# Kernel tuning notes

Hardware: AMD Instinct MI355X
Metric: run time of the kernel (lower is better)

## Reference

```python
import jax, jax.numpy as jnp
from jax import lax
import numpy as np

DN = ('NCHW', 'OIHW', 'NCHW')

def _bn(x, g, b):
    # BatchNorm2d in training mode: batch statistics, biased variance, eps=1e-5
    m = jnp.mean(x, axis=(0, 2, 3), keepdims=True)
    v = jnp.var(x, axis=(0, 2, 3), keepdims=True)
    return g[None, :, None, None] * (x - m) * lax.rsqrt(v + 1e-5) + b[None, :, None, None]

def _conv(x, w, b, s, p):
    y = lax.conv_general_dilated(x, w, (s, s), [(p, p), (p, p)], dimension_numbers=DN)
    return y + b[None, :, None, None]

def _convt(x, w, b, s, p):
    # torch ConvTranspose2d weight layout [in, out, k, k]; equivalent to
    # input-dilated conv with flipped, transposed kernel and padding k-1-p.
    k = w.shape[2]
    pp = k - 1 - p
    w2 = jnp.flip(w, (2, 3)).transpose(1, 0, 2, 3)  # [out, in, k, k]
    y = lax.conv_general_dilated(x, w2, (1, 1), [(pp, pp), (pp, pp)],
                                 lhs_dilation=(s, s), dimension_numbers=DN)
    return y + b[None, :, None, None]

def setup_inputs() -> dict:
    key = jax.random.key(0)
    ks = jax.random.split(key, 16)
    f32 = jnp.float32
    def rn(i, shape, s):
        return jax.random.normal(ks[i], shape, f32) * s
    K = 256
    inp = {
        'x': jax.random.normal(ks[0], (128, 3, 64, 64), f32),
        'codebook': jax.random.uniform(ks[1], (256, 256), f32, -1.0 / K, 1.0 / K),
        'e_w1': rn(2, (64, 3, 3, 3), 0.19), 'e_b1': jnp.zeros((64,), f32),
        'e_g1': jnp.ones((64,), f32), 'e_be1': jnp.zeros((64,), f32),
        'e_w2': rn(3, (128, 64, 4, 4), 0.031), 'e_b2': jnp.zeros((128,), f32),
        'e_g2': jnp.ones((128,), f32), 'e_be2': jnp.zeros((128,), f32),
        'e_w3': rn(4, (192, 128, 4, 4), 0.022), 'e_b3': jnp.zeros((192,), f32),
        'e_g3': jnp.ones((192,), f32), 'e_be3': jnp.zeros((192,), f32),
        'e_w4': rn(5, (256, 192, 1, 1), 0.072), 'e_b4': jnp.zeros((256,), f32),
        'd_w1': rn(6, (256, 192, 1, 1), 0.062), 'd_b1': jnp.zeros((192,), f32),
        'd_g1': jnp.ones((192,), f32), 'd_be1': jnp.zeros((192,), f32),
        'd_w2': rn(7, (192, 128, 4, 4), 0.018), 'd_b2': jnp.zeros((128,), f32),
        'd_g2': jnp.ones((128,), f32), 'd_be2': jnp.zeros((128,), f32),
        'd_w3': rn(8, (128, 64, 4, 4), 0.022), 'd_b3': jnp.zeros((64,), f32),
        'd_g3': jnp.ones((64,), f32), 'd_be3': jnp.zeros((64,), f32),
        'd_w4': rn(9, (3, 64, 3, 3), 0.042), 'd_b4': jnp.zeros((3,), f32),
    }
    return inp

def reference(x, codebook,
              e_w1, e_b1, e_g1, e_be1, e_w2, e_b2, e_g2, e_be2,
              e_w3, e_b3, e_g3, e_be3, e_w4, e_b4,
              d_w1, d_b1, d_g1, d_be1, d_w2, d_b2, d_g2, d_be2,
              d_w3, d_b3, d_g3, d_be3, d_w4, d_b4):
    # encoder
    h = jax.nn.relu(_bn(_conv(x, e_w1, e_b1, 1, 1), e_g1, e_be1))
    h = jax.nn.relu(_bn(_conv(h, e_w2, e_b2, 2, 1), e_g2, e_be2))
    h = jax.nn.relu(_bn(_conv(h, e_w3, e_b3, 2, 1), e_g3, e_be3))
    h = _conv(h, e_w4, e_b4, 1, 0)  # [B, 256, 16, 16]
    B, C, H, W = h.shape
    Z = h.transpose(0, 2, 3, 1).reshape(-1, C)  # [N, D]
    # fused cdist via ||a||^2 + ||b||^2 - 2ab (argmin invariant to const offsets)
    d2 = (jnp.sum(Z * Z, axis=1, keepdims=True)
          + jnp.sum(codebook * codebook, axis=1)[None, :]
          - 2.0 * (Z @ codebook.T))  # [N, K]
    j = jnp.argmin(d2, axis=1)
    Wj = codebook[j]  # [N, D]
    loss_commit = jnp.mean(jnp.sum((Z - lax.stop_gradient(Wj)) ** 2, axis=1))
    loss_code = jnp.mean(jnp.sum((lax.stop_gradient(Z) - Wj) ** 2, axis=1))
    hq = Wj.reshape(B, H, W, C).transpose(0, 3, 1, 2)
    # decoder
    g = jax.nn.relu(_bn(_convt(hq, d_w1, d_b1, 1, 0), d_g1, d_be1))
    g = jax.nn.relu(_bn(_convt(g, d_w2, d_b2, 2, 1), d_g2, d_be2))
    g = jax.nn.relu(_bn(_convt(g, d_w3, d_b3, 2, 1), d_g3, d_be3))
    g = _conv(g, d_w4, d_b4, 1, 1)  # [B, 3, 64, 64]
    return g, loss_commit, loss_code
```

## Files before the change

kernel.cpp:

```cpp
#include <hip/hip_runtime.h>

#define TPB 256

typedef __attribute__((ext_vector_type(4))) float v4f;
typedef __attribute__((ext_vector_type(8))) short v8s;

__device__ __forceinline__ float us2f(unsigned int u) {
    union { unsigned int i; float f; } w; w.i = u << 16; return w.f;
}
__device__ __forceinline__ unsigned short f2us(float f) {
    union { float ff; unsigned int i; } w; w.ff = f;
    unsigned int u = w.i;
    return (unsigned short)((u + 0x7fffu + ((u >> 16) & 1u)) >> 16);
}
__device__ __forceinline__ void gl_lds16(const unsigned short* g, unsigned short* l) {
    __builtin_amdgcn_global_load_lds(
        (const __attribute__((address_space(1))) unsigned int*)g,
        (__attribute__((address_space(3))) unsigned int*)l, 16, 0, 0);
}

template<int CIN, int COUT, int KK>
__global__ __launch_bounds__(TPB) void repack_w(
    const float* __restrict__ w, unsigned short* __restrict__ o)
{
    int idx = blockIdx.x * TPB + threadIdx.x;
    if (idx >= KK * COUT * CIN) return;
    int ci = idx % CIN;
    int co = (idx / CIN) % COUT;
    int kk = idx / (CIN * COUT);
    o[idx] = f2us(w[((size_t)co * CIN + ci) * KK + kk]);
}
template<int CIN, int COUT>
__global__ __launch_bounds__(TPB) void repack_wt1(
    const float* __restrict__ w, unsigned short* __restrict__ o)
{
    int idx = blockIdx.x * TPB + threadIdx.x;
    if (idx >= CIN * COUT) return;
    int ci = idx % CIN;
    int co = idx / CIN;
    o[idx] = f2us(w[(size_t)ci * COUT + co]);
}
__global__ __launch_bounds__(TPB) void repack_we1(
    const float* __restrict__ w, unsigned short* __restrict__ o)
{
    int idx = blockIdx.x * TPB + threadIdx.x;
    if (idx >= 64 * 32) return;
    int k = idx & 31, co = idx >> 5;
    o[idx] = (k < 27) ? f2us(w[co * 27 + k]) : (unsigned short)0;
}
__global__ __launch_bounds__(TPB) void repack_wd4(
    const float* __restrict__ w, unsigned short* __restrict__ o)
{
    int idx = blockIdx.x * TPB + threadIdx.x;
    if (idx >= 18 * 512) return;
    int e = idx & 7;
    int lane = (idx >> 3) & 63;
    int kk = idx >> 9;
    int lr = lane & 15, lc = lane >> 4;
    int tap = kk >> 1, half = kk & 1;
    int ci = half * 32 + lc * 8 + e;
    o[idx] = (lr < 3) ? f2us(w[((size_t)lr * 64 + ci) * 9 + tap]) : (unsigned short)0;
}
template<int CIN, int COUT, int NCB>
__global__ __launch_bounds__(TPB) void repack_wf2(
    const float* __restrict__ w, unsigned short* __restrict__ o)
{
    int idx = blockIdx.x * TPB + threadIdx.x;
    if (idx >= 16 * COUT * CIN) return;
    int e = idx & 7;
    int lane = (idx >> 3) & 63;
    int seg8 = (idx >> 9) & 7;
    int u = idx >> 12;
    int cb = u % NCB;
    int tap = u / NCB;
    int lr = lane & 15, lc = lane >> 4;
    int kc = seg8 >> 2, sg = seg8 & 3;
    int co = cb * 64 + sg * 16 + lr;
    int ci = kc * 32 + lc * 8 + e;
    o[idx] = f2us(w[((size_t)co * CIN + ci) * 16 + tap]);
}
template<int CIN, int COUT, int NCB>
__global__ __launch_bounds__(TPB) void repack_wct2(
    const float* __restrict__ w, unsigned short* __restrict__ o)
{
    constexpr int NCI = CIN / 64;
    int idx = blockIdx.x * TPB + threadIdx.x;
    if (idx >= 16 * COUT * CIN) return;
    int e = idx & 7;
    int lane = (idx >> 3) & 63;
    int seg8 = (idx >> 9) & 7;
    int u = idx >> 12;
    int cb = u % NCB;
    int u2 = u / NCB;
    int cc = u2 % NCI;
    int tk = u2 / NCI;
    int kidx = tk & 3, cls = tk >> 2;
    int lr = lane & 15, lc = lane >> 4;
    int kc = seg8 >> 2, sg = seg8 & 3;
    int co = cb * 64 + sg * 16 + lr;
    int ci = cc * 64 + kc * 32 + lc * 8 + e;
    int ohp = cls >> 1, owp = cls & 1;
    int kh = ((ohp + 1) & 1) + 2 * (kidx >> 1);
    int kw = ((owp + 1) & 1) + 2 * (kidx & 1);
    o[idx] = f2us(w[((size_t)ci * COUT + co) * 16 + kh * 4 + kw]);
}

__global__ __launch_bounds__(TPB) void im2col_e1(
    const float* __restrict__ x, unsigned short* __restrict__ A, int N)
{
    int p = blockIdx.x * TPB + threadIdx.x;
    int n = p >> 12, oh = (p >> 6) & 63, ow = p & 63;
    unsigned short row[32];
#pragma unroll
    for (int k = 0; k < 27; k++) {
        int ci = k / 9, tap = k % 9, kh = tap / 3, kw = tap % 3;
        int ih = oh - 1 + kh, iw = ow - 1 + kw;
        float v = ((unsigned)ih < 64u && (unsigned)iw < 64u)
            ? x[(((size_t)n * 3 + ci) * 64 + ih) * 64 + iw] : 0.f;
        row[k] = f2us(v);
    }
#pragma unroll
    for (int k = 27; k < 32; k++) row[k] = 0;
    int4* dst = (int4*)(A + (size_t)p * 32);
    const int4* src = (const int4*)row;
    dst[0] = src[0]; dst[1] = src[1]; dst[2] = src[2]; dst[3] = src[3];
}

__global__ __launch_bounds__(TPB) void e1_gemm(
    const unsigned short* __restrict__ A, const unsigned short* __restrict__ wrep,
    const float* __restrict__ bias, unsigned short* __restrict__ yout,
    float* __restrict__ part, int N)
{
    __shared__ __align__(16) unsigned short Ab[8 * 512];
    __shared__ __align__(16) unsigned short Bb[4 * 512];

    const int t = threadIdx.x, lane = t & 63, wave = t >> 6;
    const int wm = wave >> 1, wn = wave & 1;
    const int m0 = (int)blockIdx.x * 128;
    const int lr = lane & 15, lc = lane >> 4;

    gl_lds16(A + (size_t)(m0 + wave * 16 + lr) * 32 + lc * 8, &Ab[wave * 512]);
    gl_lds16(A + (size_t)(m0 + (wave + 4) * 16 + lr) * 32 + lc * 8, &Ab[(wave + 4) * 512]);
    gl_lds16(wrep + (size_t)(wave * 16 + lr) * 32 + lc * 8, &Bb[wave * 512]);
    __syncthreads();

    v4f acc[4][2];
#pragma unroll
    for (int i = 0; i < 4; i++)
#pragma unroll
        for (int j = 0; j < 2; j++)
#pragma unroll
            for (int r = 0; r < 4; r++) acc[i][j][r] = 0.f;

    v8s a[4], b[2];
#pragma unroll
    for (int i = 0; i < 4; i++)
        a[i] = *(const v8s*)&Ab[(wm * 4 + i) * 512 + lane * 8];
#pragma unroll
    for (int j = 0; j < 2; j++)
        b[j] = *(const v8s*)&Bb[(wn * 2 + j) * 512 + lane * 8];
#pragma unroll
    for (int i = 0; i < 4; i++)
#pragma unroll
        for (int j = 0; j < 2; j++)
            acc[i][j] = __builtin_amdgcn_mfma_f32_16x16x32_bf16(a[i], b[j], acc[i][j], 0, 0, 0);

    float sloc[2], qloc[2];
#pragma unroll
    for (int j = 0; j < 2; j++) { sloc[j] = 0.f; qloc[j] = 0.f; }

#pragma unroll
    for (int i = 0; i < 4; i++) {
        int mr = wm * 64 + i * 16 + (lane >> 4) * 4;
#pragma unroll
        for (int j = 0; j < 2; j++) {
            int col = wn * 32 + j * 16 + (lane & 15);
            float bs = bias[col];
#pragma unroll
            for (int r = 0; r < 4; r++) {
                int row = m0 + mr + r;
                int n = row >> 12, oh = (row >> 6) & 63, ow = row & 63;
                int cls = ((oh & 1) << 1) | (ow & 1);
                size_t crow = ((((size_t)cls * N + n) * 32 + (oh >> 1)) * 32 + (ow >> 1));
                float v = acc[i][j][r] + bs;
                yout[crow * 64 + col] = f2us(v);
                sloc[j] += v;
                qloc[j] += v * v;
            }
        }
    }

    __syncthreads();
    float* red = (float*)Ab;
    for (int i = t; i < 128; i += TPB) red[i] = 0.f;
    __syncthreads();
#pragma unroll
    for (int j = 0; j < 2; j++) {
        float s = sloc[j], qv = qloc[j];
        s += __shfl_xor(s, 16); s += __shfl_xor(s, 32);
        qv += __shfl_xor(qv, 16); qv += __shfl_xor(qv, 32);
        if ((lane >> 4) == 0) {
            int cl = wn * 32 + j * 16 + (lane & 15);
            atomicAdd(&red[cl], s);
            atomicAdd(&red[64 + cl], qv);
        }
    }
    __syncthreads();
    int PB = (int)gridDim.x, pb = (int)blockIdx.x;
    for (int i = t; i < 64; i += TPB) {
        part[(size_t)i * PB + pb] = red[i];
        part[(size_t)(64 + i) * PB + pb] = red[64 + i];
    }
}

template<int CIN, int COUT, int HO, int WO, int NCB>
__global__ __launch_bounds__(TPB) void conv_c(
    const unsigned short* __restrict__ xin, const unsigned short* __restrict__ wrep,
    const float* __restrict__ bias, unsigned short* __restrict__ yout,
    float* __restrict__ part, const unsigned short* __restrict__ zpage, int N)
{
    constexpr int NCI = CIN / 64;
    constexpr int NIT = 16 * NCI;
    __shared__ __align__(16) unsigned short Ab[2][16 * 1024];
    __shared__ __align__(16) unsigned short Bb[2][8 * 512];

    const int t = threadIdx.x, lane = t & 63, wave = t >> 6;
    int gdec = (int)blockIdx.x >> 3, xs = (int)blockIdx.x & 7;
    int cb = 0;
    if (NCB >= 2) { cb = gdec % NCB; gdec /= NCB; }
    const int tile = (gdec << 3) + xs;
    const int m0 = tile * 256;
    const int co0 = cb * 64;
    const int lr = lane & 15, lc = lane >> 4;

    const int jr7 = lane >> 3;
    const int sw = ((lane & 7) ^ jr7) * 8;

    int n_[4], oh_[4], ow0_[4];
#pragma unroll
    for (int q = 0; q < 4; q++) {
        int r0 = m0 + (wave * 4 + q) * 16;
        n_[q] = r0 / (HO * WO);
        int rem = r0 % (HO * WO);
        oh_[q] = rem / WO;
        ow0_[q] = rem % WO;
    }

    v4f acc[4][4];
#pragma unroll
    for (int i = 0; i < 4; i++)
#pragma unroll
        for (int j = 0; j < 4; j++)
#pragma unroll
            for (int r = 0; r < 4; r++) acc[i][j][r] = 0.f;

    auto stage = [&](int it, int buf) {
        const int tap = it / NCI, cc = it % NCI;
        const int kh = tap >> 2, kw = tap & 3;
        const int dcls = (((kh + 1) & 1) << 1) | ((kw + 1) & 1);
        const int dh2 = (kh - 1) >> 1;
        const int dw2 = (kw - 1) >> 1;
#pragma unroll
        for (int q = 0; q < 4; q++) {
            const int ih2 = oh_[q] + dh2;
            const bool ihv = (unsigned)ih2 < (unsigned)HO;
#pragma unroll
            for (int h = 0; h < 2; h++) {
                int iw2 = ow0_[q] + h * 8 + jr7 + dw2;
                bool av = ihv && (unsigned)iw2 < (unsigned)WO;
                size_t ab = ((((size_t)dcls * N + n_[q]) * HO + ih2) * WO + iw2) * CIN;
                const unsigned short* src = av ? xin + ab + cc * 64 + sw : zpage;
                gl_lds16(src, &Ab[buf][(wave * 4 + q) * 1024 + h * 512]);
            }
        }
        const unsigned short* wb = wrep
            + ((size_t)(tap * NCI + cc) * NCB + cb) * 4096;
        gl_lds16(wb + wave * 512 + lane * 8, &Bb[buf][wave * 512]);
        gl_lds16(wb + (4 + wave) * 512 + lane * 8, &Bb[buf][(4 + wave) * 512]);
    };

    auto compute = [&](int it, int buf) {
#pragma unroll
        for (int kc = 0; kc < 2; kc++) {
            v8s a[4], b[4];
#pragma unroll
            for (int i = 0; i < 4; i++)
                a[i] = *(const v8s*)&Ab[buf][(wave * 4 + i) * 1024 + lr * 64
                        + ((kc * 32 + lc * 8) ^ ((lr & 7) << 3))];
#pragma unroll
            for (int j = 0; j < 4; j++)
                b[j] = *(const v8s*)&Bb[buf][(kc * 4 + j) * 512 + lane * 8];
#pragma unroll
            for (int i = 0; i < 4; i++)
#pragma unroll
                for (int j = 0; j < 4; j++)
                    acc[i][j] = __builtin_amdgcn_mfma_f32_16x16x32_bf16(a[i], b[j], acc[i][j], 0, 0, 0);
        }
    };

    stage(0, 0);
    __syncthreads();

#pragma unroll
    for (int it = 0; it < NIT; ++it) {
        const int buf = it & 1;
        if (it + 1 < NIT) stage(it + 1, buf ^ 1);
        compute(it, buf);
        __syncthreads();
    }

    float sloc[4], qloc[4];
#pragma unroll
    for (int j = 0; j < 4; j++) { sloc[j] = 0.f; qloc[j] = 0.f; }

#pragma unroll
    for (int i = 0; i < 4; i++) {
        int mr = wave * 64 + i * 16 + (lane >> 4) * 4;
#pragma unroll
        for (int j = 0; j < 4; j++) {
            int col = co0 + j * 16 + (lane & 15);
            float bs = bias[col];
#pragma unroll
            for (int r = 0; r < 4; r++) {
                size_t gi = (size_t)(m0 + mr + r) * COUT + col;
                float v = acc[i][j][r] + bs;
                yout[gi] = f2us(v);
                sloc[j] += v;
                qloc[j] += v * v;
            }
        }
    }

    float* red = (float*)Ab;
    for (int i = t; i < 128; i += TPB) red[i] = 0.f;
    __syncthreads();
#pragma unroll
    for (int j = 0; j < 4; j++) {
        float s = sloc[j], qv = qloc[j];
        s += __shfl_xor(s, 16); s += __shfl_xor(s, 32);
        qv += __shfl_xor(qv, 16); qv += __shfl_xor(qv, 32);
        if ((lane >> 4) == 0) {
            int cl = j * 16 + (lane & 15);
            atomicAdd(&red[cl], s);
            atomicAdd(&red[64 + cl], qv);
        }
    }
    __syncthreads();
    const int TILES = (N * HO * WO) >> 8;
    const int pb = tile;
    for (int i = t; i < 64; i += TPB) {
        part[(size_t)(co0 + i) * TILES + pb] = red[i];
        part[(size_t)(COUT + co0 + i) * TILES + pb] = red[64 + i];
    }
}

template<int CIN, int COUT, int HIN, int WIN, int K, int S, int P, int BN,
         int OUTM, int NYB>
__global__ __launch_bounds__(TPB) void conv_mfma(
    const unsigned short* __restrict__ xin, const unsigned short* __restrict__ wrep,
    const float* __restrict__ bias, void* __restrict__ yout, void* __restrict__ yout2,
    float* __restrict__ part, const unsigned short* __restrict__ zpage, int N)
{
    constexpr int HOUT = (HIN + 2 * P - K) / S + 1;
    constexpr int WOUT = (WIN + 2 * P - K) / S + 1;
    constexpr int RN = BN / 32;
    constexpr int BSEG = BN / 16;
    constexpr int NCI = CIN / 64;
    constexpr int NIT = K * K * NCI;
    __shared__ __align__(16) unsigned short Ab[2][16 * 512];
    __shared__ __align__(16) unsigned short Bb[2][2 * BSEG * 512];

    const int t = threadIdx.x, lane = t & 63, wave = t >> 6;
    const int wm = wave >> 1, wn = wave & 1;
    int m0, co0;
    if (NYB == 2) {
        int g = (int)blockIdx.x >> 3, xs = (int)blockIdx.x & 7;
        co0 = (g & 1) * BN;
        m0 = (((g >> 1) << 3) + xs) * 128;
    } else {
        m0 = (int)blockIdx.x * 128;
        co0 = 0;
    }
    const int lr = lane & 15, lc = lane >> 4;

    int n_[2], oh_[2], ow_[2];
#pragma unroll
    for (int i = 0; i < 2; i++) {
        int r = m0 + (wave + 4 * i) * 16 + lr;
        n_[i] = r / (HOUT * WOUT);
        int rem = r % (HOUT * WOUT);
        oh_[i] = rem / WOUT;
        ow_[i] = rem % WOUT;
    }

    v4f acc[4][RN];
#pragma unroll
    for (int i = 0; i < 4; i++)
#pragma unroll
        for (int j = 0; j < RN; j++)
#pragma unroll
            for (int r = 0; r < 4; r++) acc[i][j][r] = 0.f;

    auto do_stage = [&](int it, int pb) {
        const int kk = it / NCI;
        const int ci0 = (it % NCI) * 64;
        const int kh = kk / K, kw = kk % K;
#pragma unroll
        for (int i = 0; i < 2; i++) {
            int ih = oh_[i] * S - P + kh;
            int iw = ow_[i] * S - P + kw;
            bool av = (unsigned)ih < (unsigned)HIN && (unsigned)iw < (unsigned)WIN;
            const unsigned short* b0 = av
                ? xin + (((size_t)n_[i] * HIN + ih) * WIN + iw) * CIN + lc * 8 + ci0
                : zpage;
            gl_lds16(b0, &Ab[pb][(wave + 4 * i) * 512]);
            gl_lds16(av ? b0 + 32 : zpage, &Ab[pb][(8 + wave + 4 * i) * 512]);
        }
        const unsigned short* wt = wrep + (size_t)kk * COUT * CIN;
#pragma unroll
        for (int i = 0; i < 2; i++) {
            int sgb = wave + 4 * i;
            if (sgb < BSEG) {
                const unsigned short* wb =
                    wt + (size_t)(co0 + sgb * 16 + lr) * CIN + ci0 + lc * 8;
                gl_lds16(wb, &Bb[pb][sgb * 512]);
                gl_lds16(wb + 32, &Bb[pb][(BSEG + sgb) * 512]);
            }
        }
    };

    do_stage(0, 0);
    __syncthreads();

    for (int it = 0; it < NIT; ++it) {
        const int pb = it & 1;
        if (it + 1 < NIT) do_stage(it + 1, pb ^ 1);

#pragma unroll
        for (int kc = 0; kc < 2; kc++) {
            v8s a[4], b[RN];
#pragma unroll
            for (int i = 0; i < 4; i++)
                a[i] = *(const v8s*)&Ab[pb][(kc * 8 + wm * 4 + i) * 512 + lane * 8];
#pragma unroll
            for (int j = 0; j < RN; j++)
                b[j] = *(const v8s*)&Bb[pb][(kc * BSEG + wn * RN + j) * 512 + lane * 8];
#pragma unroll
            for (int i = 0; i < 4; i++)
#pragma unroll
                for (int j = 0; j < RN; j++)
                    acc[i][j] = __builtin_amdgcn_mfma_f32_16x16x32_bf16(a[i], b[j], acc[i][j], 0, 0, 0);
        }
        __syncthreads();
    }

    float sloc[RN], qloc[RN];
#pragma unroll
    for (int j = 0; j < RN; j++) { sloc[j] = 0.f; qloc[j] = 0.f; }

#pragma unroll
    for (int i = 0; i < 4; i++) {
        int mr = wm * 64 + i * 16 + (lane >> 4) * 4;
#pragma unroll
        for (int j = 0; j < RN; j++) {
            int col = co0 + wn * (BN / 2) + j * 16 + (lane & 15);
            float bs = bias[col];
#pragma unroll
            for (int r = 0; r < 4; r++) {
                size_t g = (size_t)(m0 + mr + r) * COUT + col;
                float v = acc[i][j][r] + bs;
                if (OUTM == 2) {
                    unsigned short h = f2us(v);
                    ((unsigned short*)yout)[g] = h;
                    ((unsigned short*)yout2)[g] = f2us(v - us2f(h));
                } else {
                    ((unsigned short*)yout)[g] = f2us(v);
                    sloc[j] += v;
                    qloc[j] += v * v;
                }
            }
        }
    }

    if (OUTM == 0) {
        __syncthreads();
        float* red = (float*)Ab;
        for (int i = t; i < 2 * BN; i += TPB) red[i] = 0.f;
        __syncthreads();
#pragma unroll
        for (int j = 0; j < RN; j++) {
            float s = sloc[j], qv = qloc[j];
            s += __shfl_xor(s, 16); s += __shfl_xor(s, 32);
            qv += __shfl_xor(qv, 16); qv += __shfl_xor(qv, 32);
            if ((lane >> 4) == 0) {
                int cl = wn * (BN / 2) + j * 16 + (lane & 15);
                atomicAdd(&red[cl], s);
                atomicAdd(&red[BN + cl], qv);
            }
        }
        __syncthreads();
        int pb = (NYB == 2) ? (m0 >> 7) : (int)blockIdx.x;
        int PB = (NYB == 2) ? ((int)gridDim.x >> 1) : (int)gridDim.x;
        for (int i = t; i < BN; i += TPB) {
            int col = co0 + i;
            part[(size_t)col * PB + pb] = red[i];
            part[(size_t)(COUT + col) * PB + pb] = red[BN + i];
        }
    }
}

template<int CIN, int COUT, int HIN, int WIN, int NCB, int IN_CLS>
__global__ __launch_bounds__(TPB) void convt_c(
    const unsigned short* __restrict__ xin, const unsigned short* __restrict__ wrep,
    const float* __restrict__ bias, unsigned short* __restrict__ yout,
    float* __restrict__ part, const unsigned short* __restrict__ zpage, int N)
{
    constexpr int NCI = CIN / 64;
    constexpr int NIT = 4 * NCI;
    __shared__ __align__(16) unsigned short Ab[2][16 * 1024];
    __shared__ __align__(16) unsigned short Bb[2][8 * 512];

    const int t = threadIdx.x, lane = t & 63, wave = t >> 6;
    int gdec = (int)blockIdx.x >> 3, xs = (int)blockIdx.x & 7;
    int cb = 0;
    if (NCB == 2) { cb = gdec & 1; gdec >>= 1; }
    const int cls = gdec & 3;
    const int tile = ((gdec >> 2) << 3) + xs;
    const int m0 = tile * 256;
    const int co0 = cb * 64;
    const int ohp = cls >> 1, owp = cls & 1;
    const int khb = (ohp + 1) & 1, kwb = (owp + 1) & 1;
    const int dh0 = (ohp + 1 - khb) >> 1, dw0 = (owp + 1 - kwb) >> 1;
    const int lr = lane & 15, lc = lane >> 4;

    const int jr7 = lane >> 3;
    const int sw = ((lane & 7) ^ jr7) * 8;

    int n_[4], i_[4], j0_[4];
#pragma unroll
    for (int q = 0; q < 4; q++) {
        int r0 = m0 + (wave * 4 + q) * 16;
        n_[q] = r0 / (HIN * WIN);
        int rem = r0 % (HIN * WIN);
        i_[q] = rem / WIN;
        j0_[q] = rem % WIN;
    }

    v4f acc[4][4];
#pragma unroll
    for (int i = 0; i < 4; i++)
#pragma unroll
        for (int j = 0; j < 4; j++)
#pragma unroll
            for (int r = 0; r < 4; r++) acc[i][j][r] = 0.f;

    auto stage = [&](int it, int buf) {
        const int tap = it / NCI, cc = it % NCI;
        const int dh = dh0 - (tap >> 1);
        const int dw = dw0 - (tap & 1);
#pragma unroll
        for (int q = 0; q < 4; q++) {
            const int ih = i_[q] + dh;
            const bool ihv = (unsigned)ih < (unsigned)HIN;
#pragma unroll
            for (int h = 0; h < 2; h++) {
                int iw = j0_[q] + h * 8 + jr7 + dw;
                bool av = ihv && (unsigned)iw < (unsigned)WIN;
                size_t ab;
                if (IN_CLS) {
                    int clsi = ((ih & 1) << 1) | (iw & 1);
                    ab = ((((size_t)clsi * N + n_[q]) * (HIN / 2) + (ih >> 1)) * (WIN / 2)
                         + (iw >> 1)) * CIN;
                } else {
                    ab = (((size_t)n_[q] * HIN + ih) * WIN + iw) * CIN;
                }
                const unsigned short* src = av ? xin + ab + cc * 64 + sw : zpage;
                gl_lds16(src, &Ab[buf][(wave * 4 + q) * 1024 + h * 512]);
            }
        }
        const unsigned short* wb = wrep
            + ((size_t)((cls * 4 + tap) * NCI + cc) * NCB + cb) * 4096;
        gl_lds16(wb + wave * 512 + lane * 8, &Bb[buf][wave * 512]);
        gl_lds16(wb + (4 + wave) * 512 + lane * 8, &Bb[buf][(4 + wave) * 512]);
    };

    auto compute = [&](int it, int buf) {
#pragma unroll
        for (int kc = 0; kc < 2; kc++) {
            v8s a[4], b[4];
#pragma unroll
            for (int i = 0; i < 4; i++)
                a[i] = *(const v8s*)&Ab[buf][(wave * 4 + i) * 1024 + lr * 64
                        + ((kc * 32 + lc * 8) ^ ((lr & 7) << 3))];
#pragma unroll
            for (int j = 0; j < 4; j++)
                b[j] = *(const v8s*)&Bb[buf][(kc * 4 + j) * 512 + lane * 8];
#pragma unroll
            for (int i = 0; i < 4; i++)
#pragma unroll
                for (int j = 0; j < 4; j++)
                    acc[i][j] = __builtin_amdgcn_mfma_f32_16x16x32_bf16(a[i], b[j], acc[i][j], 0, 0, 0);
        }
    };

    stage(0, 0);
    __syncthreads();

#pragma unroll
    for (int it = 0; it < NIT; ++it) {
        const int buf = it & 1;
        if (it + 1 < NIT) stage(it + 1, buf ^ 1);
        compute(it, buf);
        __syncthreads();
    }

    float sloc[4], qloc[4];
#pragma unroll
    for (int j = 0; j < 4; j++) { sloc[j] = 0.f; qloc[j] = 0.f; }

    const size_t clsbase = (size_t)cls * N * HIN * WIN;
#pragma unroll
    for (int i = 0; i < 4; i++) {
        int mr = wave * 64 + i * 16 + (lane >> 4) * 4;
#pragma unroll
        for (int j = 0; j < 4; j++) {
            int col = co0 + j * 16 + (lane & 15);
            float bs = bias[col];
#pragma unroll
            for (int r = 0; r < 4; r++) {
                size_t gi = (clsbase + m0 + mr + r) * COUT + col;
                float v = acc[i][j][r] + bs;
                yout[gi] = f2us(v);
                sloc[j] += v;
                qloc[j] += v * v;
            }
        }
    }

    float* red = (float*)Ab;
    for (int i = t; i < 128; i += TPB) red[i] = 0.f;
    __syncthreads();
#pragma unroll
    for (int j = 0; j < 4; j++) {
        float s = sloc[j], qv = qloc[j];
        s += __shfl_xor(s, 16); s += __shfl_xor(s, 32);
        qv += __shfl_xor(qv, 16); qv += __shfl_xor(qv, 32);
        if ((lane >> 4) == 0) {
            int cl = j * 16 + (lane & 15);
            atomicAdd(&red[cl], s);
            atomicAdd(&red[64 + cl], qv);
        }
    }
    __syncthreads();
    const int TILES = (N * HIN * WIN) >> 8;
    const int PB = 4 * TILES;
    const int pb = cls * TILES + tile;
    for (int i = t; i < 64; i += TPB) {
        part[(size_t)(co0 + i) * PB + pb] = red[i];
        part[(size_t)(COUT + co0 + i) * PB + pb] = red[64 + i];
    }
}

template<int C>
__global__ __launch_bounds__(64) void bn_reduce2(
    const float* __restrict__ part, float* __restrict__ st, int B)
{
    int i = blockIdx.x;
    int lane = threadIdx.x;
    float s = 0.f;
    for (int b = lane; b < B; b += 64) s += part[(size_t)i * B + b];
#pragma unroll
    for (int off = 1; off < 64; off <<= 1) s += __shfl_xor(s, off);
    if (lane == 0) st[i] = s;
}

template<int C>
__global__ __launch_bounds__(TPB) void bn_apply_v(
    unsigned short* __restrict__ x, const float* __restrict__ st,
    const float* __restrict__ g, const float* __restrict__ be, int M)
{
    __shared__ float sc[C], sh[C];
    int t = threadIdx.x;
    float cnt = (float)M;
    for (int c = t; c < C; c += TPB) {
        float m = st[c] / cnt;
        float v = st[C + c] / cnt - m * m;
        float s = g[c] * rsqrtf(v + 1e-5f);
        sc[c] = s;
        sh[c] = be[c] - m * s;
    }
    __syncthreads();
    constexpr int GPT = C / 8;
    size_t tot = (size_t)M * GPT;
    for (size_t slot = (size_t)blockIdx.x * TPB + t; slot < tot;
         slot += (size_t)gridDim.x * TPB) {
        int c0 = (int)(slot % GPT) * 8;
        int4 v = *(int4*)(x + slot * 8);
        unsigned int* vu = (unsigned int*)&v;
#pragma unroll
        for (int k = 0; k < 4; k++) {
            float f0 = fmaxf(us2f(vu[k] & 0xffffu) * sc[c0 + 2 * k] + sh[c0 + 2 * k], 0.f);
            float f1 = fmaxf(us2f(vu[k] >> 16) * sc[c0 + 2 * k + 1] + sh[c0 + 2 * k + 1], 0.f);
            vu[k] = (unsigned int)f2us(f0) | ((unsigned int)f2us(f1) << 16);
        }
        *(int4*)(x + slot * 8) = v;
    }
}

__global__ __launch_bounds__(TPB) void cb_prep(
    const float* __restrict__ cb, unsigned short* __restrict__ chb,
    unsigned short* __restrict__ clb, float* __restrict__ cn2)
{
    int j = blockIdx.x, d = threadIdx.x;
    float v = cb[j * 256 + d];
    unsigned short h = f2us(v);
    chb[j * 256 + d] = h;
    clb[j * 256 + d] = f2us(v - us2f(h));
    float s = v * v;
#pragma unroll
    for (int off = 1; off < 64; off <<= 1) s += __shfl_xor(s, off);
    __shared__ float p[4];
    if ((d & 63) == 0) p[d >> 6] = s;
    __syncthreads();
    if (d == 0) cn2[j] = p[0] + p[1] + p[2] + p[3];
}

__global__ __launch_bounds__(TPB) void vq_gemm(
    const unsigned short* __restrict__ zh, const unsigned short* __restrict__ zl,
    const unsigned short* __restrict__ chb, const unsigned short* __restrict__ clb,
    const float* __restrict__ cn2, float* __restrict__ valp, int* __restrict__ idxp)
{
    __shared__ __align__(16) unsigned short Ah[2][8 * 512];
    __shared__ __align__(16) unsigned short Al[2][8 * 512];
    __shared__ __align__(16) unsigned short Bh[2][8 * 512];
    __shared__ __align__(16) unsigned short Bl[2][8 * 512];

    const int t = threadIdx.x, lane = t & 63, wave = t >> 6;
    const int wm = wave >> 1, wn = wave & 1;
    const int gdec = (int)blockIdx.x >> 3, xs = (int)blockIdx.x & 7;
    const int cbk = gdec & 1;
    const int m0 = (((gdec >> 1) << 3) + xs) * 128;
    const int co0 = cbk * 128;
    const int lr = lane & 15, lc = lane >> 4;

    size_t a0 = (size_t)(m0 + wave * 16 + lr) * 256 + lc * 8;
    size_t a1 = a0 + 64 * 256;
    size_t b0 = (size_t)(co0 + wave * 16 + lr) * 256 + lc * 8;
    size_t b1 = b0 + 64 * 256;

    v4f acc[4][4];
#pragma unroll
    for (int i = 0; i < 4; i++)
#pragma unroll
        for (int j = 0; j < 4; j++)
#pragma unroll
            for (int r = 0; r < 4; r++) acc[i][j][r] = 0.f;

    auto do_stage = [&](int ci0, int pb) {
        gl_lds16(zh + a0 + ci0, &Ah[pb][wave * 512]);
        gl_lds16(zh + a1 + ci0, &Ah[pb][(wave + 4) * 512]);
        gl_lds16(zl + a0 + ci0, &Al[pb][wave * 512]);
        gl_lds16(zl + a1 + ci0, &Al[pb][(wave + 4) * 512]);
        gl_lds16(chb + b0 + ci0, &Bh[pb][wave * 512]);
        gl_lds16(chb + b1 + ci0, &Bh[pb][(wave + 4) * 512]);
        gl_lds16(clb + b0 + ci0, &Bl[pb][wave * 512]);
        gl_lds16(clb + b1 + ci0, &Bl[pb][(wave + 4) * 512]);
    };

    do_stage(0, 0);
    __syncthreads();

    for (int s = 0; s < 8; ++s) {
        const int pb = s & 1;
        if (s < 7) do_stage((s + 1) * 32, pb ^ 1);

        v8s a_h[4], a_l[4], b_h[4], b_l[4];
#pragma unroll
        for (int i = 0; i < 4; i++) {
            a_h[i] = *(const v8s*)&Ah[pb][(wm * 4 + i) * 512 + lane * 8];
            a_l[i] = *(const v8s*)&Al[pb][(wm * 4 + i) * 512 + lane * 8];
        }
#pragma unroll
        for (int j = 0; j < 4; j++) {
            b_h[j] = *(const v8s*)&Bh[pb][(wn * 4 + j) * 512 + lane * 8];
            b_l[j] = *(const v8s*)&Bl[pb][(wn * 4 + j) * 512 + lane * 8];
        }
#pragma unroll
        for (int i = 0; i < 4; i++)
#pragma unroll
            for (int j = 0; j < 4; j++) {
                acc[i][j] = __builtin_amdgcn_mfma_f32_16x16x32_bf16(a_h[i], b_h[j], acc[i][j], 0, 0, 0);
                acc[i][j] = __builtin_amdgcn_mfma_f32_16x16x32_bf16(a_h[i], b_l[j], acc[i][j], 0, 0, 0);
                acc[i][j] = __builtin_amdgcn_mfma_f32_16x16x32_bf16(a_l[i], b_h[j], acc[i][j], 0, 0, 0);
            }
        __syncthreads();
    }

#pragma unroll
    for (int i = 0; i < 4; i++) {
#pragma unroll
        for (int r = 0; r < 4; r++) {
            float best = 3.4e38f;
            int bi = 0;
#pragma unroll
            for (int j = 0; j < 4; j++) {
                int col = co0 + wn * 64 + j * 16 + (lane & 15);
                float d = cn2[col] - 2.f * acc[i][j][r];
                if (d < best || (d == best && col < bi)) { best = d; bi = col; }
            }
#pragma unroll
            for (int off = 1; off < 16; off <<= 1) {
                float ov = __shfl_xor(best, off);
                int oi = __shfl_xor(bi, off);
                if (ov < best || (ov == best && oi < bi)) { best = ov; bi = oi; }
            }
            if ((lane & 15) == 0) {
                int row = m0 + wm * 64 + i * 16 + (lane >> 4) * 4 + r;
                valp[(size_t)row * 4 + cbk * 2 + wn] = best;
                idxp[(size_t)row * 4 + cbk * 2 + wn] = bi;
            }
        }
    }
}

__global__ __launch_bounds__(TPB) void vq_gather2(
    const unsigned short* __restrict__ zh, const unsigned short* __restrict__ zl,
    const float* __restrict__ cb, const float* __restrict__ valp,
    const int* __restrict__ idxp, unsigned short* __restrict__ hq,
    float* __restrict__ rowloss)
{
    int row = blockIdx.x * 4 + (threadIdx.x >> 6);
    int lane = threadIdx.x & 63;
    float best = valp[(size_t)row * 4];
    int j = idxp[(size_t)row * 4];
#pragma unroll
    for (int c = 1; c < 4; c++) {
        float v = valp[(size_t)row * 4 + c];
        if (v < best) { best = v; j = idxp[(size_t)row * 4 + c]; }
    }
    ushort4 hv = *(const ushort4*)(zh + (size_t)row * 256 + lane * 4);
    ushort4 lv = *(const ushort4*)(zl + (size_t)row * 256 + lane * 4);
    float4 cv = *(const float4*)(cb + (size_t)j * 256 + lane * 4);
    float z0 = us2f(hv.x) + us2f(lv.x);
    float z1 = us2f(hv.y) + us2f(lv.y);
    float z2 = us2f(hv.z) + us2f(lv.z);
    float z3 = us2f(hv.w) + us2f(lv.w);
    float d0 = z0 - cv.x, d1 = z1 - cv.y, d2 = z2 - cv.z, d3 = z3 - cv.w;
    float d = d0 * d0 + d1 * d1 + d2 * d2 + d3 * d3;
#pragma unroll
    for (int off = 1; off < 64; off <<= 1) d += __shfl_xor(d, off);
    if (lane == 0) rowloss[row] = d;
    ushort4 o;
    o.x = f2us(cv.x); o.y = f2us(cv.y); o.z = f2us(cv.z); o.w = f2us(cv.w);
    *(ushort4*)(hq + (size_t)row * 256 + lane * 4) = o;
}

__global__ __launch_bounds__(TPB) void loss_reduce1(
    const float* __restrict__ rowloss, float* __restrict__ part64)
{
    int t = threadIdx.x;
    int base = blockIdx.x * 512 + t;
    float v = rowloss[base] + rowloss[base + 256];
#pragma unroll
    for (int off = 1; off < 64; off <<= 1) v += __shfl_xor(v, off);
    __shared__ float p[4];
    if ((t & 63) == 0) p[t >> 6] = v;
    __syncthreads();
    if (t == 0) part64[blockIdx.x] = p[0] + p[1] + p[2] + p[3];
}

__global__ __launch_bounds__(64) void loss_finalize(
    const float* __restrict__ part64, float* __restrict__ out2)
{
    float v = part64[threadIdx.x];
    for (int off = 32; off > 0; off >>= 1) v += __shfl_down(v, off);
    if (threadIdx.x == 0) {
        float m = v * (1.0f / 32768.0f);
        out2[0] = m;
        out2[1] = m;
    }
}

__global__ __launch_bounds__(TPB) void conv_d4(
    const unsigned short* __restrict__ xb, const unsigned short* __restrict__ wrep,
    const float* __restrict__ bias, float* __restrict__ out, int N)
{
    __shared__ __align__(16) unsigned short xsm[8 * 409 * 8];
    int4* xsI = (int4*)xsm;
    const int t = threadIdx.x;
    const int lane = t & 63, wave = t >> 6;
    const int lr = lane & 15, lc = lane >> 4;

    const int n = blockIdx.x >> 4;
    const int tile = blockIdx.x & 15;
    const int th = tile >> 2, tw = tile & 3;
    const int ihh0 = 8 * th - 1, iwh0 = 8 * tw - 1;

    for (int s = t; s < 3200; s += TPB) {
        int cls = s / 800;
        int rem = s % 800;
        int ihh_l = rem / 80;
        int i4 = rem % 80;
        int iwh_l = i4 >> 3, c8 = i4 & 7;
        int ihh_g = ihh0 + ihh_l;
        int iwh_g = iwh0 + iwh_l;
        int4 v;
        if ((unsigned)ihh_g < 32u && (unsigned)iwh_g < 32u) {
            size_t row = (((size_t)cls * 128 + n) * 32 + ihh_g) * 32 + iwh_g;
            v = *(const int4*)(xb + row * 64 + c8 * 8);
        } else {
            v.x = v.y = v.z = v.w = 0;
        }
        xsI[c8 * 409 + cls * 102 + ihh_l * 10 + iwh_l] = v;
    }
    __syncthreads();

    int abase[4][9];
#pragma unroll
    for (int q = 0; q < 4; q++) {
        int seg = wave * 4 + q;
        int oh = th * 16 + seg;
        int ow = tw * 16 + lr;
#pragma unroll
        for (int tap = 0; tap < 9; tap++) {
            int kh = tap / 3, kw = tap % 3;
            int ih = oh - 1 + kh, iw = ow - 1 + kw;
            int clsi = ((ih & 1) << 1) | (iw & 1);
            abase[q][tap] = clsi * 102 + ((ih >> 1) - ihh0) * 10 + ((iw >> 1) - iwh0);
        }
    }

    v4f acc[4];
#pragma unroll
    for (int q = 0; q < 4; q++)
#pragma unroll
        for (int r = 0; r < 4; r++) acc[q][r] = 0.f;

#pragma unroll
    for (int kk = 0; kk < 18; kk++) {
        const int tap = kk >> 1, half = kk & 1;
        const int c8 = half * 4 + lc;
        v8s b = *(const v8s*)(wrep + kk * 512 + lane * 8);
#pragma unroll
        for (int q = 0; q < 4; q++) {
            v8s a = *(const v8s*)&xsI[c8 * 409 + abase[q][tap]];
            acc[q] = __builtin_amdgcn_mfma_f32_16x16x32_bf16(a, b, acc[q], 0, 0, 0);
        }
    }

    if (lr < 3) {
        float bs = bias[lr];
#pragma unroll
        for (int q = 0; q < 4; q++) {
            int seg = wave * 4 + q;
            int oh = th * 16 + seg;
            int ow0 = tw * 16 + lc * 4;
            float4 v;
            v.x = acc[q][0] + bs; v.y = acc[q][1] + bs;
            v.z = acc[q][2] + bs; v.w = acc[q][3] + bs;
            *(float4*)&out[((size_t)n * 3 + lr) * 4096 + oh * 64 + ow0] = v;
        }
    }
}


extern "C" void kernel_launch(void* const* d_in, const int* in_sizes, int n_in,
                              void* d_out, int out_size, void* d_ws, size_t ws_size,
                              hipStream_t stream) {
    const float* x    = (const float*)d_in[0];
    const float* cb   = (const float*)d_in[1];
    const float* e_w1 = (const float*)d_in[2];  const float* e_b1 = (const float*)d_in[3];
    const float* e_g1 = (const float*)d_in[4];  const float* e_be1 = (const float*)d_in[5];
    const float* e_w2 = (const float*)d_in[6];  const float* e_b2 = (const float*)d_in[7];
    const float* e_g2 = (const float*)d_in[8];  const float* e_be2 = (const float*)d_in[9];
    const float* e_w3 = (const float*)d_in[10]; const float* e_b3 = (const float*)d_in[11];
    const float* e_g3 = (const float*)d_in[12]; const float* e_be3 = (const float*)d_in[13];
    const float* e_w4 = (const float*)d_in[14]; const float* e_b4 = (const float*)d_in[15];
    const float* d_w1 = (const float*)d_in[16]; const float* d_b1 = (const float*)d_in[17];
    const float* d_g1 = (const float*)d_in[18]; const float* d_be1 = (const float*)d_in[19];
    const float* d_w2 = (const float*)d_in[20]; const float* d_b2 = (const float*)d_in[21];
    const float* d_g2 = (const float*)d_in[22]; const float* d_be2 = (const float*)d_in[23];
    const float* d_w3 = (const float*)d_in[24]; const float* d_b3 = (const float*)d_in[25];
    const float* d_g3 = (const float*)d_in[26]; const float* d_be3 = (const float*)d_in[27];
    const float* d_w4 = (const float*)d_in[28]; const float* d_b4 = (const float*)d_in[29];

    float* ws = (float*)d_ws;
    unsigned short* h1 = (unsigned short*)(ws);
    unsigned short* g3 = h1;
    unsigned short* h2 = (unsigned short*)(ws + 16777216);
    unsigned short* g2 = h2;
    unsigned short* h3 = (unsigned short*)(ws + 25165824);
    unsigned short* g1 = h3;
    unsigned short* zh = (unsigned short*)(ws + 28311552);
    unsigned short* zl = (unsigned short*)(ws + 32505856);
    unsigned short* aim = zh;
    unsigned short* hq = (unsigned short*)(ws + 36700160);
    float* stats = ws + 40960000;
    unsigned short* we1 = (unsigned short*)(ws + 40963072);
    unsigned short* wd4r = (unsigned short*)(ws + 40964096);
    float* cn2 = ws + 40995904;
    unsigned short* chb = (unsigned short*)(ws + 40996160);
    unsigned short* clb = (unsigned short*)(ws + 41028928);
    unsigned short* wrep = (unsigned short*)(ws + 41061696);
    unsigned short* we2 = wrep + 0;
    unsigned short* we3 = wrep + 131072;
    unsigned short* we4 = wrep + 524288;
    unsigned short* wd1 = wrep + 573440;
    unsigned short* wd2 = wrep + 622592;
    unsigned short* wd3 = wrep + 1015808;
    float* part = ws + 41635136;
    float* valp = part;
    int* idxp = (int*)(part + 131072);
    float* rowloss = ws + 50023744;
    float* part64 = ws + 50122048;
    unsigned short* zpage = (unsigned short*)(ws + 50122112);
    float* out = (float*)d_out;
    float* losses = out + 1572864;

    const int N = 128;

    hipMemsetAsync(zpage, 0, 256, stream);

    repack_we1<<<8, TPB, 0, stream>>>(e_w1, we1);
    repack_wd4<<<36, TPB, 0, stream>>>(d_w4, wd4r);
    repack_wf2<64, 128, 2><<<512, TPB, 0, stream>>>(e_w2, we2);
    repack_w<128, 192, 16><<<1536, TPB, 0, stream>>>(e_w3, we3);
    repack_w<192, 256, 1><<<192, TPB, 0, stream>>>(e_w4, we4);
    repack_wt1<256, 192><<<192, TPB, 0, stream>>>(d_w1, wd1);
    repack_wct2<192, 128, 2><<<1536, TPB, 0, stream>>>(d_w2, wd2);
    repack_wct2<128, 64, 1><<<512, TPB, 0, stream>>>(d_w3, wd3);
    cb_prep<<<256, TPB, 0, stream>>>(cb, chb, clb, cn2);

    im2col_e1<<<2048, TPB, 0, stream>>>(x, aim, N);
    e1_gemm<<<4096, TPB, 0, stream>>>(aim, we1, e_b1, h1, part, N);
    bn_reduce2<64><<<128, 64, 0, stream>>>(part, stats + 0 * 512, 4096);
    bn_apply_v<64><<<4096, TPB, 0, stream>>>(h1, stats + 0 * 512, e_g1, e_be1, 524288);

    conv_c<64, 128, 32, 32, 2>
        <<<1024, TPB, 0, stream>>>(h1, we2, e_b2, h2, part, zpage, N);
    bn_reduce2<128><<<256, 64, 0, stream>>>(part, stats + 1 * 512, 512);
    bn_apply_v<128><<<2048, TPB, 0, stream>>>(h2, stats + 1 * 512, e_g2, e_be2, 131072);

    conv_mfma<128, 192, 32, 32, 4, 2, 1, 96, 0, 2>
        <<<512, TPB, 0, stream>>>(h2, we3, e_b3, h3, nullptr, part, zpage, N);
    bn_reduce2<192><<<384, 64, 0, stream>>>(part, stats + 2 * 512, 256);
    bn_apply_v<192><<<1024, TPB, 0, stream>>>(h3, stats + 2 * 512, e_g3, e_be3, 32768);

    conv_mfma<192, 256, 16, 16, 1, 1, 0, 128, 2, 2>
        <<<512, TPB, 0, stream>>>(h3, we4, e_b4, zh, zl, nullptr, zpage, N);

    vq_gemm<<<512, TPB, 0, stream>>>(zh, zl, chb, clb, cn2, valp, idxp);
    vq_gather2<<<8192, TPB, 0, stream>>>(zh, zl, cb, valp, idxp, hq, rowloss);
    loss_reduce1<<<64, TPB, 0, stream>>>(rowloss, part64);
    loss_finalize<<<1, 64, 0, stream>>>(part64, losses);

    conv_mfma<256, 192, 16, 16, 1, 1, 0, 96, 0, 2>
        <<<512, TPB, 0, stream>>>(hq, wd1, d_b1, g1, nullptr, part, zpage, N);
    bn_reduce2<192><<<384, 64, 0, stream>>>(part, stats + 3 * 512, 256);
    bn_apply_v<192><<<1024, TPB, 0, stream>>>(g1, stats + 3 * 512, d_g1, d_be1, 32768);

    convt_c<192, 128, 16, 16, 2, 0>
        <<<1024, TPB, 0, stream>>>(g1, wd2, d_b2, g2, part, zpage, N);
    bn_reduce2<128><<<256, 64, 0, stream>>>(part, stats + 4 * 512, 512);
    bn_apply_v<128><<<2048, TPB, 0, stream>>>(g2, stats + 4 * 512, d_g2, d_be2, 131072);

    convt_c<128, 64, 32, 32, 1, 1>
        <<<2048, TPB, 0, stream>>>(g2, wd3, d_b3, g3, part, zpage, N);
    bn_reduce2<64><<<128, 64, 0, stream>>>(part, stats + 5 * 512, 2048);
    bn_apply_v<64><<<4096, TPB, 0, stream>>>(g3, stats + 5 * 512, d_g3, d_be3, 524288);

    conv_d4<<<2048, TPB, 0, stream>>>(g3, wd4r, d_b4, out, N);
}
```

Before: 666.9 us.

## Fuse weight repacks into one kernel, fold last BN+ReLU into conv_d4, merge loss reduction

Merges the eight weight-repack kernels and the zero-page memset into a single launch, and folds the two-stage loss reduction into one single-block kernel. It also removes the separate bn_apply pass over g3 by applying the BN scale/shift and ReLU inside conv_d4's tile load. This cuts launch overhead and one full read-write pass over the largest decoder activation. The cost is redundant per-block BN parameter computation, extra ALU work in the conv_d4 load loop, and a serial single-block loss sum over 32768 values.

```diff
diff --git a/kernel.cpp b/kernel.cpp
--- a/kernel.cpp
+++ b/kernel.cpp
@@ -19,90 +19,121 @@
         (__attribute__((address_space(3))) unsigned int*)l, 16, 0, 0);
 }
 
-template<int CIN, int COUT, int KK>
-__global__ __launch_bounds__(TPB) void repack_w(
-    const float* __restrict__ w, unsigned short* __restrict__ o)
-{
-    int idx = blockIdx.x * TPB + threadIdx.x;
-    if (idx >= KK * COUT * CIN) return;
-    int ci = idx % CIN;
-    int co = (idx / CIN) % COUT;
-    int kk = idx / (CIN * COUT);
-    o[idx] = f2us(w[((size_t)co * CIN + ci) * KK + kk]);
-}
-template<int CIN, int COUT>
-__global__ __launch_bounds__(TPB) void repack_wt1(
-    const float* __restrict__ w, unsigned short* __restrict__ o)
-{
-    int idx = blockIdx.x * TPB + threadIdx.x;
-    if (idx >= CIN * COUT) return;
-    int ci = idx % CIN;
-    int co = idx / CIN;
-    o[idx] = f2us(w[(size_t)ci * COUT + co]);
-}
-__global__ __launch_bounds__(TPB) void repack_we1(
-    const float* __restrict__ w, unsigned short* __restrict__ o)
-{
-    int idx = blockIdx.x * TPB + threadIdx.x;
-    if (idx >= 64 * 32) return;
-    int k = idx & 31, co = idx >> 5;
-    o[idx] = (k < 27) ? f2us(w[co * 27 + k]) : (unsigned short)0;
-}
-__global__ __launch_bounds__(TPB) void repack_wd4(
-    const float* __restrict__ w, unsigned short* __restrict__ o)
-{
-    int idx = blockIdx.x * TPB + threadIdx.x;
-    if (idx >= 18 * 512) return;
-    int e = idx & 7;
-    int lane = (idx >> 3) & 63;
-    int kk = idx >> 9;
-    int lr = lane & 15, lc = lane >> 4;
-    int tap = kk >> 1, half = kk & 1;
-    int ci = half * 32 + lc * 8 + e;
-    o[idx] = (lr < 3) ? f2us(w[((size_t)lr * 64 + ci) * 9 + tap]) : (unsigned short)0;
-}
-template<int CIN, int COUT, int NCB>
-__global__ __launch_bounds__(TPB) void repack_wf2(
-    const float* __restrict__ w, unsigned short* __restrict__ o)
-{
-    int idx = blockIdx.x * TPB + threadIdx.x;
-    if (idx >= 16 * COUT * CIN) return;
-    int e = idx & 7;
-    int lane = (idx >> 3) & 63;
-    int seg8 = (idx >> 9) & 7;
-    int u = idx >> 12;
-    int cb = u % NCB;
-    int tap = u / NCB;
-    int lr = lane & 15, lc = lane >> 4;
-    int kc = seg8 >> 2, sg = seg8 & 3;
-    int co = cb * 64 + sg * 16 + lr;
-    int ci = kc * 32 + lc * 8 + e;
-    o[idx] = f2us(w[((size_t)co * CIN + ci) * 16 + tap]);
-}
-template<int CIN, int COUT, int NCB>
-__global__ __launch_bounds__(TPB) void repack_wct2(
-    const float* __restrict__ w, unsigned short* __restrict__ o)
-{
-    constexpr int NCI = CIN / 64;
-    int idx = blockIdx.x * TPB + threadIdx.x;
-    if (idx >= 16 * COUT * CIN) return;
-    int e = idx & 7;
-    int lane = (idx >> 3) & 63;
-    int seg8 = (idx >> 9) & 7;
-    int u = idx >> 12;
-    int cb = u % NCB;
-    int u2 = u / NCB;
-    int cc = u2 % NCI;
-    int tk = u2 / NCI;
-    int kidx = tk & 3, cls = tk >> 2;
-    int lr = lane & 15, lc = lane >> 4;
-    int kc = seg8 >> 2, sg = seg8 & 3;
-    int co = cb * 64 + sg * 16 + lr;
-    int ci = cc * 64 + kc * 32 + lc * 8 + e;
-    int ohp = cls >> 1, owp = cls & 1;
-    int kh = ((ohp + 1) & 1) + 2 * (kidx >> 1);
-    int kw = ((owp + 1) & 1) + 2 * (kidx & 1);
-    o[idx] = f2us(w[((size_t)ci * COUT + co) * 16 + kh * 4 + kw]);
+__global__ __launch_bounds__(TPB) void repack_all(
+    const float* __restrict__ e_w1, const float* __restrict__ d_w4,
+    const float* __restrict__ e_w2, const float* __restrict__ e_w3,
+    const float* __restrict__ e_w4, const float* __restrict__ d_w1,
+    const float* __restrict__ d_w2, const float* __restrict__ d_w3,
+    unsigned short* __restrict__ we1, unsigned short* __restrict__ wd4r,
+    unsigned short* __restrict__ we2, unsigned short* __restrict__ we3,
+    unsigned short* __restrict__ we4, unsigned short* __restrict__ wd1,
+    unsigned short* __restrict__ wd2, unsigned short* __restrict__ wd3,
+    unsigned short* __restrict__ zpage)
+{
+    int gid = blockIdx.x * TPB + threadIdx.x;
+    if (gid < 2048) {
+        int idx = gid;
+        int k = idx & 31, co = idx >> 5;
+        we1[idx] = (k < 27) ? f2us(e_w1[co * 27 + k]) : (unsigned short)0;
+        return;
+    }
+    gid -= 2048;
+    if (gid < 9216) {
+        int idx = gid;
+        int e = idx & 7;
+        int lane = (idx >> 3) & 63;
+        int kk = idx >> 9;
+        int lr = lane & 15, lc = lane >> 4;
+        int tap = kk >> 1, half = kk & 1;
+        int ci = half * 32 + lc * 8 + e;
+        wd4r[idx] = (lr < 3) ? f2us(d_w4[((size_t)lr * 64 + ci) * 9 + tap])
+                             : (unsigned short)0;
+        return;
+    }
+    gid -= 9216;
+    if (gid < 131072) {
+        int idx = gid;
+        int e = idx & 7;
+        int lane = (idx >> 3) & 63;
+        int seg8 = (idx >> 9) & 7;
+        int u = idx >> 12;
+        int cb = u % 2, tap = u / 2;
+        int lr = lane & 15, lc = lane >> 4;
+        int kc = seg8 >> 2, sg = seg8 & 3;
+        int co = cb * 64 + sg * 16 + lr;
+        int ci = kc * 32 + lc * 8 + e;
+        we2[idx] = f2us(e_w2[((size_t)co * 64 + ci) * 16 + tap]);
+        return;
+    }
+    gid -= 131072;
+    if (gid < 393216) {
+        int idx = gid;
+        int ci = idx % 128;
+        int co = (idx / 128) % 192;
+        int kk = idx / (128 * 192);
+        we3[idx] = f2us(e_w3[((size_t)co * 128 + ci) * 16 + kk]);
+        return;
+    }
+    gid -= 393216;
+    if (gid < 49152) {
+        int idx = gid;
+        int ci = idx % 192;
+        int co = (idx / 192) % 256;
+        we4[idx] = f2us(e_w4[(size_t)co * 192 + ci]);
+        return;
+    }
+    gid -= 49152;
+    if (gid < 49152) {
+        int idx = gid;
+        int ci = idx % 256;
+        int co = idx / 256;
+        wd1[idx] = f2us(d_w1[(size_t)ci * 192 + co]);
+        return;
+    }
+    gid -= 49152;
+    if (gid < 393216) {
+        int idx = gid;
+        int e = idx & 7;
+        int lane = (idx >> 3) & 63;
+        int seg8 = (idx >> 9) & 7;
+        int u = idx >> 12;
+        int cb = u % 2;
+        int u2 = u / 2;
+        int cc = u2 % 3;
+        int tk = u2 / 3;
+        int kidx = tk & 3, cls = tk >> 2;
+        int lr = lane & 15, lc = lane >> 4;
+        int kc = seg8 >> 2, sg = seg8 & 3;
+        int co = cb * 64 + sg * 16 + lr;
+        int ci = cc * 64 + kc * 32 + lc * 8 + e;
+        int ohp = cls >> 1, owp = cls & 1;
+        int kh = ((ohp + 1) & 1) + 2 * (kidx >> 1);
+        int kw = ((owp + 1) & 1) + 2 * (kidx & 1);
+        wd2[idx] = f2us(d_w2[((size_t)ci * 128 + co) * 16 + kh * 4 + kw]);
+        return;
+    }
+    gid -= 393216;
+    if (gid < 131072) {
+        int idx = gid;
+        int e = idx & 7;
+        int lane = (idx >> 3) & 63;
+        int seg8 = (idx >> 9) & 7;
+        int u2 = idx >> 12;
+        int cc = u2 % 2;
+        int tk = u2 / 2;
+        int kidx = tk & 3, cls = tk >> 2;
+        int lr = lane & 15, lc = lane >> 4;
+        int kc = seg8 >> 2, sg = seg8 & 3;
+        int co = sg * 16 + lr;
+        int ci = cc * 64 + kc * 32 + lc * 8 + e;
+        int ohp = cls >> 1, owp = cls & 1;
+        int kh = ((ohp + 1) & 1) + 2 * (kidx >> 1);
+        int kw = ((owp + 1) & 1) + 2 * (kidx & 1);
+        wd3[idx] = f2us(d_w3[((size_t)ci * 64 + co) * 16 + kh * 4 + kw]);
+        return;
+    }
+    gid -= 131072;
+    if (gid < 128) zpage[gid] = 0;
 }
 
 __global__ __launch_bounds__(TPB) void im2col_e1(
@@ -855,27 +886,19 @@
     *(ushort4*)(hq + (size_t)row * 256 + lane * 4) = o;
 }
 
-__global__ __launch_bounds__(TPB) void loss_reduce1(
-    const float* __restrict__ rowloss, float* __restrict__ part64)
+__global__ __launch_bounds__(TPB) void loss_all(
+    const float* __restrict__ rowloss, float* __restrict__ out2)
 {
     int t = threadIdx.x;
-    int base = blockIdx.x * 512 + t;
-    float v = rowloss[base] + rowloss[base + 256];
+    float v = 0.f;
+    for (int i = t; i < 32768; i += TPB) v += rowloss[i];
 #pragma unroll
     for (int off = 1; off < 64; off <<= 1) v += __shfl_xor(v, off);
     __shared__ float p[4];
     if ((t & 63) == 0) p[t >> 6] = v;
     __syncthreads();
-    if (t == 0) part64[blockIdx.x] = p[0] + p[1] + p[2] + p[3];
-}
-
-__global__ __launch_bounds__(64) void loss_finalize(
-    const float* __restrict__ part64, float* __restrict__ out2)
-{
-    float v = part64[threadIdx.x];
-    for (int off = 32; off > 0; off >>= 1) v += __shfl_down(v, off);
-    if (threadIdx.x == 0) {
-        float m = v * (1.0f / 32768.0f);
+    if (t == 0) {
+        float m = (p[0] + p[1] + p[2] + p[3]) * (1.0f / 32768.0f);
         out2[0] = m;
         out2[1] = m;
     }
@@ -883,13 +906,26 @@
 
 __global__ __launch_bounds__(TPB) void conv_d4(
     const unsigned short* __restrict__ xb, const unsigned short* __restrict__ wrep,
-    const float* __restrict__ bias, float* __restrict__ out, int N)
+    const float* __restrict__ st, const float* __restrict__ gg,
+    const float* __restrict__ be, const float* __restrict__ bias,
+    float* __restrict__ out, int N)
 {
     __shared__ __align__(16) unsigned short xsm[8 * 409 * 8];
+    __shared__ float scs[64], shs[64];
     int4* xsI = (int4*)xsm;
     const int t = threadIdx.x;
     const int lane = t & 63, wave = t >> 6;
     const int lr = lane & 15, lc = lane >> 4;
+
+    if (t < 64) {
+        float cnt = (float)(N * 4096);
+        float m = st[t] / cnt;
+        float vv = st[64 + t] / cnt - m * m;
+        float s = gg[t] * rsqrtf(vv + 1e-5f);
+        scs[t] = s;
+        shs[t] = be[t] - m * s;
+    }
+    __syncthreads();
 
     const int n = blockIdx.x >> 4;
     const int tile = blockIdx.x & 15;
@@ -908,6 +944,14 @@
         if ((unsigned)ihh_g < 32u && (unsigned)iwh_g < 32u) {
             size_t row = (((size_t)cls * 128 + n) * 32 + ihh_g) * 32 + iwh_g;
             v = *(const int4*)(xb + row * 64 + c8 * 8);
+            unsigned int* vu = (unsigned int*)&v;
+            int c0 = c8 * 8;
+#pragma unroll
+            for (int k = 0; k < 4; k++) {
+                float f0 = fmaxf(us2f(vu[k] & 0xffffu) * scs[c0 + 2 * k] + shs[c0 + 2 * k], 0.f);
+                float f1 = fmaxf(us2f(vu[k] >> 16) * scs[c0 + 2 * k + 1] + shs[c0 + 2 * k + 1], 0.f);
+                vu[k] = (unsigned int)f2us(f0) | ((unsigned int)f2us(f1) << 16);
+            }
         } else {
             v.x = v.y = v.z = v.w = 0;
         }
@@ -1016,19 +1060,13 @@
     unsigned short* zpage = (unsigned short*)(ws + 50122112);
     float* out = (float*)d_out;
     float* losses = out + 1572864;
+    (void)part64;
 
     const int N = 128;
 
-    hipMemsetAsync(zpage, 0, 256, stream);
-
-    repack_we1<<<8, TPB, 0, stream>>>(e_w1, we1);
-    repack_wd4<<<36, TPB, 0, stream>>>(d_w4, wd4r);
-    repack_wf2<64, 128, 2><<<512, TPB, 0, stream>>>(e_w2, we2);
-    repack_w<128, 192, 16><<<1536, TPB, 0, stream>>>(e_w3, we3);
-    repack_w<192, 256, 1><<<192, TPB, 0, stream>>>(e_w4, we4);
-    repack_wt1<256, 192><<<192, TPB, 0, stream>>>(d_w1, wd1);
-    repack_wct2<192, 128, 2><<<1536, TPB, 0, stream>>>(d_w2, wd2);
-    repack_wct2<128, 64, 1><<<512, TPB, 0, stream>>>(d_w3, wd3);
+    repack_all<<<4525, TPB, 0, stream>>>(
+        e_w1, d_w4, e_w2, e_w3, e_w4, d_w1, d_w2, d_w3,
+        we1, wd4r, we2, we3, we4, wd1, wd2, wd3, zpage);
     cb_prep<<<256, TPB, 0, stream>>>(cb, chb, clb, cn2);
 
     im2col_e1<<<2048, TPB, 0, stream>>>(x, aim, N);
@@ -1051,8 +1089,7 @@
 
     vq_gemm<<<512, TPB, 0, stream>>>(zh, zl, chb, clb, cn2, valp, idxp);
     vq_gather2<<<8192, TPB, 0, stream>>>(zh, zl, cb, valp, idxp, hq, rowloss);
-    loss_reduce1<<<64, TPB, 0, stream>>>(rowloss, part64);
-    loss_finalize<<<1, 64, 0, stream>>>(part64, losses);
+    loss_all<<<1, TPB, 0, stream>>>(rowloss, losses);
 
     conv_mfma<256, 192, 16, 16, 1, 1, 0, 96, 0, 2>
         <<<512, TPB, 0, stream>>>(hq, wd1, d_b1, g1, nullptr, part, zpage, N);
@@ -1067,7 +1104,7 @@
     convt_c<128, 64, 32, 32, 1, 1>
         <<<2048, TPB, 0, stream>>>(g2, wd3, d_b3, g3, part, zpage, N);
     bn_reduce2<64><<<128, 64, 0, stream>>>(part, stats + 5 * 512, 2048);
-    bn_apply_v<64><<<4096, TPB, 0, stream>>>(g3, stats + 5 * 512, d_g3, d_be3, 524288);
-
-    conv_d4<<<2048, TPB, 0, stream>>>(g3, wd4r, d_b4, out, N);
-}
+
+    conv_d4<<<2048, TPB, 0, stream>>>(g3, wd4r, stats + 5 * 512, d_g3, d_be3,
+                                      d_b4, out, N);
+}
```

New measurement: 582.2 us. 1.15x faster.
